# Optimization experiments

Measured on AMD Instinct MI355X. Metric: run time of the kernel, lower is better.

Reference implementation:

```python
import jax, jax.numpy as jnp
import numpy as np

N_NODES = 100000
N_EDGES = 1600000
IN_CH = 128
OUT_CH = 128

def setup_inputs() -> dict:
    key = jax.random.key(0)
    k1, k2, k3, k4, k5 = jax.random.split(key, 5)
    x = jax.random.normal(k1, (N_NODES, IN_CH), dtype=jnp.float32)
    src = jax.random.randint(k2, (N_EDGES,), 0, N_NODES, dtype=jnp.int64)
    dst = jax.random.randint(k3, (N_EDGES,), 0, N_NODES, dtype=jnp.int64)
    edge_index = jnp.stack([src, dst], axis=0)
    W = jax.random.normal(k4, (OUT_CH, IN_CH), dtype=jnp.float32) * (1.0 / np.sqrt(IN_CH))
    b = jax.random.normal(k5, (OUT_CH,), dtype=jnp.float32) * 0.01
    return {"x": x, "edge_index": edge_index, "W": W, "b": b}

def reference(x, edge_index, W, b):
    n = x.shape[0]
    src, dst = edge_index[0], edge_index[1]
    loop = jnp.arange(n, dtype=edge_index.dtype)
    src_all = jnp.concatenate([src, loop])  # [E+N]
    dst_all = jnp.concatenate([dst, loop])  # [E+N]
    # in-degree (with self loops) per node
    deg = jax.ops.segment_sum(jnp.ones_like(dst_all, dtype=x.dtype), dst_all, num_segments=n)
    norm = (deg[src_all] * deg[dst_all]) ** -0.5
    norm = jnp.where(jnp.isinf(norm), 0.0, norm)
    h = x @ W.T + b  # [N, out_ch]
    msg = h[src_all] * norm[:, None]  # [E+N, out_ch]
    out = jax.ops.segment_sum(msg, dst_all, num_segments=n)  # [N, out_ch]
    return out
```

## Files before the change

### kernel.cpp

```cpp
#include <hip/hip_runtime.h>
#include <hip/hip_bf16.h>


#define N_NODES 100000
#define N_EDGES 1600000
#define CH 128
#define NC 49
#define CAPC 34816
#define NCHUNK 17
#define NFB 1563
#define FCAP 1280

using bf16x8 = __attribute__((ext_vector_type(8))) short;
using f32x4  = __attribute__((ext_vector_type(4))) float;

__device__ inline unsigned short f2bf(float f) {
    unsigned u = __float_as_uint(f);
    u += 0x7fffu + ((u >> 16) & 1u);
    return (unsigned short)(u >> 16);
}
__device__ inline float bflo(unsigned u) { return __uint_as_float(u << 16); }
__device__ inline float bfhi(unsigned u) { return __uint_as_float(u & 0xffff0000u); }

__global__ __launch_bounds__(256) void k_sortA(const int* __restrict__ src,
                                               const int* __restrict__ dst,
                                               int* __restrict__ ctail,
                                               unsigned* __restrict__ E1) {
    __shared__ int hist[NC];
    __shared__ int boff[NC + 1];
    __shared__ int cur[NC];
    __shared__ int gb[NC];
    __shared__ unsigned stage[2048];
    const int t    = threadIdx.x;
    const int base = blockIdx.x * 2048;
    const int n    = min(2048, N_EDGES - base);

    if (t < NC) hist[t] = 0;
    __syncthreads();

    int s[8], d[8];
#pragma unroll
    for (int h = 0; h < 2; ++h) {
        int idx = h * 1024 + 4 * t;
        if (idx < n) {
            int4 sv = *(const int4*)&src[base + idx];
            int4 dv = *(const int4*)&dst[base + idx];
            s[4*h+0] = sv.x; s[4*h+1] = sv.y; s[4*h+2] = sv.z; s[4*h+3] = sv.w;
            d[4*h+0] = dv.x; d[4*h+1] = dv.y; d[4*h+2] = dv.z; d[4*h+3] = dv.w;
        } else {
            d[4*h+0] = d[4*h+1] = d[4*h+2] = d[4*h+3] = -1;
            s[4*h+0] = s[4*h+1] = s[4*h+2] = s[4*h+3] = 0;
        }
    }
#pragma unroll
    for (int j = 0; j < 8; ++j)
        if (d[j] >= 0) atomicAdd(&hist[d[j] >> 11], 1);
    __syncthreads();

    if (t < NC) gb[t] = atomicAdd(&ctail[t], hist[t]);
    if (t == 0) {
        int run = 0;
        for (int k = 0; k < NC; ++k) { boff[k] = run; run += hist[k]; }
        boff[NC] = run;
    }
    __syncthreads();
    if (t < NC) cur[t] = boff[t];
    __syncthreads();

#pragma unroll
    for (int j = 0; j < 8; ++j)
        if (d[j] >= 0) {
            int k = d[j] >> 11;
            int pos = atomicAdd(&cur[k], 1);
            stage[pos] = ((unsigned)s[j] << 11) | (unsigned)(d[j] & 2047);
        }
    __syncthreads();

    const int tot = boff[NC];
    for (int i = t; i < tot; i += 256) {
        int lo = 0, hi = NC;
#pragma unroll
        for (int it = 0; it < 6; ++it) {
            int mid = (lo + hi) >> 1;
            bool c = (boff[mid] <= i);
            lo = c ? mid : lo;
            hi = c ? hi : mid;
        }
        int p = gb[lo] + (i - boff[lo]);
        if (p < CAPC) E1[(size_t)lo * CAPC + p] = stage[i];
    }
}

__global__ __launch_bounds__(256) void k_sortB(const unsigned* __restrict__ E1,
                                               const int* __restrict__ ctail,
                                               int* __restrict__ ftail,
                                               unsigned* __restrict__ E2) {
    __shared__ int hist[32];
    __shared__ int boff[33];
    __shared__ int cur[32];
    __shared__ int gb[32];
    __shared__ unsigned stage[2048];
    const int cb = blockIdx.x / NCHUNK;
    const int ch = blockIdx.x % NCHUNK;
    const int t  = threadIdx.x;
    int cnt = ctail[cb]; if (cnt > CAPC) cnt = CAPC;
    const int begin = ch * 2048;
    int n = cnt - begin;
    if (n <= 0) return;
    if (n > 2048) n = 2048;
    const unsigned* e1 = E1 + (size_t)cb * CAPC + begin;

    if (t < 32) hist[t] = 0;
    __syncthreads();

    for (int i = t; i < n; i += 256)
        atomicAdd(&hist[(e1[i] >> 6) & 31], 1);
    __syncthreads();

    if (t < 32) gb[t] = atomicAdd(&ftail[cb * 32 + t], hist[t]);
    if (t == 0) {
        int run = 0;
        for (int k = 0; k < 32; ++k) { boff[k] = run; run += hist[k]; }
        boff[32] = run;
    }
    __syncthreads();
    if (t < 32) cur[t] = boff[t];
    __syncthreads();

    for (int i = t; i < n; i += 256) {
        unsigned v = e1[i];
        int k = (v >> 6) & 31;
        int pos = atomicAdd(&cur[k], 1);
        stage[pos] = ((v >> 11) << 6) | (v & 63);
    }
    __syncthreads();

    const int tot = boff[32];
    for (int i = t; i < tot; i += 256) {
        int lo = 0, hi = 32;
#pragma unroll
        for (int it = 0; it < 5; ++it) {
            int mid = (lo + hi) >> 1;
            bool c = (boff[mid] <= i);
            lo = c ? mid : lo;
            hi = c ? hi : mid;
        }
        int p = gb[lo] + (i - boff[lo]);
        int fb = cb * 32 + lo;
        if (p < FCAP) E2[(size_t)fb * FCAP + p] = stage[i];
    }
}

__global__ __launch_bounds__(256) void k_deg(const unsigned* __restrict__ E2,
                                             const int* __restrict__ ftail,
                                             float* __restrict__ rinv) {
    __shared__ int bins[64];
    const int fb = blockIdx.x;
    const int t  = threadIdx.x;
    if (t < 64) bins[t] = 0;
    int n = ftail[fb]; if (n > FCAP) n = FCAP;
    __syncthreads();
    const unsigned* e2 = E2 + (size_t)fb * FCAP;
    for (int i = t; i < n; i += 256) atomicAdd(&bins[e2[i] & 63], 1);
    __syncthreads();
    if (t < 64) {
        int node = fb * 64 + t;
        if (node < N_NODES) rinv[node] = rsqrtf((float)(bins[t] + 1));
    }
}

__device__ inline void cvt8(const float4 a, const float4 b, bf16x8& h, bf16x8& l) {
    bf16x8 H, L;
#define CV(i, f) { unsigned short hb = f2bf(f); H[i] = (short)hb;               \
                   L[i] = (short)f2bf((f) - __uint_as_float((unsigned)hb << 16)); }
    CV(0, a.x) CV(1, a.y) CV(2, a.z) CV(3, a.w)
    CV(4, b.x) CV(5, b.y) CV(6, b.z) CV(7, b.w)
#undef CV
    h = H; l = L;
}

#define MFMA(a, b, c) __builtin_amdgcn_mfma_f32_16x16x32_bf16((a), (b), (c), 0, 0, 0)

__global__ __launch_bounds__(256) void k_gemm(const float* __restrict__ x,
                                              const float* __restrict__ W,
                                              const float* __restrict__ b,
                                              const float* __restrict__ rinv,
                                              unsigned short* __restrict__ hs) {
    __shared__ __align__(16) unsigned short wh[CH * CH];
    __shared__ __align__(16) unsigned short wl[CH * CH];
    const int t = threadIdx.x;

    for (int c = t; c < 2048; c += 256) {
        int o   = c >> 4;
        int kk  = (c & 15) << 3;
        const float* wp = &W[(size_t)o * CH + kk];
        float4 w0 = *(const float4*)wp;
        float4 w1 = *(const float4*)(wp + 4);
        bf16x8 H, L;
        cvt8(w0, w1, H, L);
        unsigned boff = ((unsigned)((o << 8) | (kk << 1))) ^ ((unsigned)(o & 7) << 4);
        *(bf16x8*)((char*)wh + boff) = H;
        *(bf16x8*)((char*)wl + boff) = L;
    }
    __syncthreads();

    const int lane = t & 63;
    const int l15  = lane & 15;
    const int lhi  = lane >> 4;
    const int kc   = lhi << 3;
    const int row_base = blockIdx.x * 128 + (t >> 6) * 32;

    int r0 = row_base + l15;       if (r0 > N_NODES - 1) r0 = N_NODES - 1;
    int r1 = row_base + 16 + l15;  if (r1 > N_NODES - 1) r1 = N_NODES - 1;
    const float* x0 = &x[(size_t)r0 * CH + kc];
    const float* x1 = &x[(size_t)r1 * CH + kc];

    float4 xa[4][2], xb[4][2];
#pragma unroll
    for (int ks = 0; ks < 4; ++ks) {
        xa[ks][0] = *(const float4*)(x0 + ks * 32);
        xa[ks][1] = *(const float4*)(x0 + ks * 32 + 4);
        xb[ks][0] = *(const float4*)(x1 + ks * 32);
        xb[ks][1] = *(const float4*)(x1 + ks * 32 + 4);
    }

    f32x4 acc[2][8];
#pragma unroll
    for (int rf = 0; rf < 2; ++rf)
#pragma unroll
        for (int cf = 0; cf < 8; ++cf)
            acc[rf][cf] = (f32x4){0.f, 0.f, 0.f, 0.f};

#pragma unroll
    for (int ks = 0; ks < 4; ++ks) {
        bf16x8 ah0, al0, ah1, al1;
        cvt8(xa[ks][0], xa[ks][1], ah0, al0);
        cvt8(xb[ks][0], xb[ks][1], ah1, al1);
        const unsigned kb = (unsigned)((ks * 32 + kc) << 1);
#pragma unroll
        for (int cf = 0; cf < 8; ++cf) {
            int o = cf * 16 + l15;
            unsigned boff = (((unsigned)(o << 8)) + kb) ^ ((unsigned)(o & 7) << 4);
            bf16x8 bh = *(const bf16x8*)((const char*)wh + boff);
            bf16x8 bl = *(const bf16x8*)((const char*)wl + boff);
            acc[0][cf] = MFMA(ah0, bh, acc[0][cf]);
            acc[1][cf] = MFMA(ah1, bh, acc[1][cf]);
            acc[0][cf] = MFMA(al0, bh, acc[0][cf]);
            acc[1][cf] = MFMA(al1, bh, acc[1][cf]);
            acc[0][cf] = MFMA(ah0, bl, acc[0][cf]);
            acc[1][cf] = MFMA(ah1, bl, acc[1][cf]);
        }
    }

    float bcol[8];
#pragma unroll
    for (int cf = 0; cf < 8; ++cf) bcol[cf] = b[cf * 16 + l15];

#pragma unroll
    for (int rf = 0; rf < 2; ++rf) {
        int rb = row_base + rf * 16 + lhi * 4;
        if (rb >= N_NODES) continue;
        float4 ri4 = *(const float4*)&rinv[rb];
        float ri[4] = {ri4.x, ri4.y, ri4.z, ri4.w};
#pragma unroll
        for (int j = 0; j < 4; ++j) {
            size_t ro = (size_t)(rb + j) * CH;
#pragma unroll
            for (int cf = 0; cf < 8; ++cf)
                hs[ro + cf * 16 + l15] = f2bf(ri[j] * (acc[rf][cf][j] + bcol[cf]));
        }
    }
}

#define ACC8(u)                                                            \
    do {                                                                   \
        acc[0] += bflo((u).x); acc[1] += bfhi((u).x);                      \
        acc[2] += bflo((u).y); acc[3] += bfhi((u).y);                      \
        acc[4] += bflo((u).z); acc[5] += bfhi((u).z);                      \
        acc[6] += bflo((u).w); acc[7] += bfhi((u).w);                      \
    } while (0)

__global__ __launch_bounds__(256) void k_spmm(const unsigned* __restrict__ E2,
                                              const int* __restrict__ ftail,
                                              const float* __restrict__ rinv,
                                              const unsigned short* __restrict__ hs,
                                              float* __restrict__ out) {
    __shared__ int bins[64];
    __shared__ int boff[65];
    __shared__ int cur[64];
    __shared__ int srt[FCAP];
    const int fb    = blockIdx.x;
    const int node0 = fb * 64;
    const int t     = threadIdx.x;
    const unsigned* e2 = E2 + (size_t)fb * FCAP;
    const uint4* hp = (const uint4*)hs;

    if (t < 64) bins[t] = 0;
    int n = ftail[fb]; if (n > FCAP) n = FCAP;
    __syncthreads();

    for (int i = t; i < n; i += 256) atomicAdd(&bins[e2[i] & 63], 1);
    __syncthreads();

    if (t == 0) {
        int run = 0;
        for (int k = 0; k < 64; ++k) { boff[k] = run; run += bins[k]; }
        boff[64] = run;
    }
    __syncthreads();
    if (t < 64) cur[t] = boff[t];
    __syncthreads();

    for (int i = t; i < n; i += 256) {
        unsigned v = e2[i];
        int pos = atomicAdd(&cur[v & 63], 1);
        srt[pos] = (int)(v >> 6);
    }
    __syncthreads();

    const int grp  = t >> 4;
    const int lane = t & 15;
#pragma unroll
    for (int r = 0; r < 4; ++r) {
        const int nl   = grp * 4 + r;
        const int node = node0 + nl;
        if (node >= N_NODES) continue;
        float acc[8] = {};
        {
            uint4 u = hp[(size_t)node * 16 + lane];
            ACC8(u);
        }
        int e  = boff[nl];
        int e1 = boff[nl + 1];
        for (; e + 8 <= e1; e += 8) {
            int s0 = srt[e + 0], s1 = srt[e + 1], s2 = srt[e + 2], s3 = srt[e + 3];
            int s4 = srt[e + 4], s5 = srt[e + 5], s6 = srt[e + 6], s7 = srt[e + 7];
            uint4 u0 = hp[(size_t)s0 * 16 + lane];
            uint4 u1 = hp[(size_t)s1 * 16 + lane];
            uint4 u2 = hp[(size_t)s2 * 16 + lane];
            uint4 u3 = hp[(size_t)s3 * 16 + lane];
            uint4 u4 = hp[(size_t)s4 * 16 + lane];
            uint4 u5 = hp[(size_t)s5 * 16 + lane];
            uint4 u6 = hp[(size_t)s6 * 16 + lane];
            uint4 u7 = hp[(size_t)s7 * 16 + lane];
            ACC8(u0); ACC8(u1); ACC8(u2); ACC8(u3);
            ACC8(u4); ACC8(u5); ACC8(u6); ACC8(u7);
        }
        for (; e + 4 <= e1; e += 4) {
            int s0 = srt[e + 0];
            int s1 = srt[e + 1];
            int s2 = srt[e + 2];
            int s3 = srt[e + 3];
            uint4 u0 = hp[(size_t)s0 * 16 + lane];
            uint4 u1 = hp[(size_t)s1 * 16 + lane];
            uint4 u2 = hp[(size_t)s2 * 16 + lane];
            uint4 u3 = hp[(size_t)s3 * 16 + lane];
            ACC8(u0); ACC8(u1); ACC8(u2); ACC8(u3);
        }
        for (; e < e1; ++e) {
            uint4 u = hp[(size_t)srt[e] * 16 + lane];
            ACC8(u);
        }
        float ri = rinv[node];
        f32x4 o0, o1;
        o0[0] = ri * acc[0]; o0[1] = ri * acc[1]; o0[2] = ri * acc[2]; o0[3] = ri * acc[3];
        o1[0] = ri * acc[4]; o1[1] = ri * acc[5]; o1[2] = ri * acc[6]; o1[3] = ri * acc[7];
        __builtin_nontemporal_store(o0, (f32x4*)&out[(size_t)node * CH + lane * 8]);
        __builtin_nontemporal_store(o1, (f32x4*)&out[(size_t)node * CH + lane * 8 + 4]);
    }
}

extern "C" void kernel_launch(void* const* d_in, const int* in_sizes, int n_in,
                              void* d_out, int out_size, void* d_ws, size_t ws_size,
                              hipStream_t stream) {
    const float* x  = (const float*)d_in[0];
    const int*   ei = (const int*)d_in[1];
    const float* W  = (const float*)d_in[2];
    const float* b  = (const float*)d_in[3];
    float* out = (float*)d_out;

    const int* src = ei;
    const int* dst = ei + N_EDGES;

    int*      ctail = (int*)d_ws;
    int*      ftail = ctail + 64;
    float*    rinv  = (float*)(ftail + 1600);
    unsigned* E1    = (unsigned*)(rinv + N_NODES);
    unsigned* E2    = E1 + (size_t)NC * CAPC;
    unsigned short* hs = (unsigned short*)(E2 + (size_t)NFB * FCAP);

    hipMemsetAsync(ctail, 0, (64 + 1600) * sizeof(int), stream);

    k_sortA<<<(N_EDGES + 2047) / 2048, 256, 0, stream>>>(src, dst, ctail, E1);
    k_sortB<<<NC * NCHUNK, 256, 0, stream>>>(E1, ctail, ftail, E2);
    k_deg<<<NFB, 256, 0, stream>>>(E2, ftail, rinv);
    k_gemm<<<(N_NODES + 127) / 128, 256, 0, stream>>>(x, W, b, rinv, hs);
    k_spmm<<<NFB, 256, 0, stream>>>(E2, ftail, rinv, hs, out);
}
```

Before: 231.9 us.

## Fuse degree count into sort kernels and balance SpMM rows by degree

```diff
diff --git a/kernel.cpp b/kernel.cpp
--- a/kernel.cpp
+++ b/kernel.cpp
@@ -25,7 +25,8 @@
 __global__ __launch_bounds__(256) void k_sortA(const int* __restrict__ src,
                                                const int* __restrict__ dst,
                                                int* __restrict__ ctail,
-                                               unsigned* __restrict__ E1) {
+                                               unsigned* __restrict__ E1,
+                                               int* __restrict__ deg) {
     __shared__ int hist[NC];
     __shared__ int boff[NC + 1];
     __shared__ int cur[NC];
@@ -54,7 +55,10 @@
     }
 #pragma unroll
     for (int j = 0; j < 8; ++j)
-        if (d[j] >= 0) atomicAdd(&hist[d[j] >> 11], 1);
+        if (d[j] >= 0) {
+            atomicAdd(&hist[d[j] >> 11], 1);
+            atomicAdd(&deg[d[j]], 1);
+        }
     __syncthreads();
 
     if (t < NC) gb[t] = atomicAdd(&ctail[t], hist[t]);
@@ -94,7 +98,9 @@
 __global__ __launch_bounds__(256) void k_sortB(const unsigned* __restrict__ E1,
                                                const int* __restrict__ ctail,
                                                int* __restrict__ ftail,
-                                               unsigned* __restrict__ E2) {
+                                               unsigned* __restrict__ E2,
+                                               const int* __restrict__ deg,
+                                               float* __restrict__ rinv) {
     __shared__ int hist[32];
     __shared__ int boff[33];
     __shared__ int cur[32];
@@ -103,6 +109,12 @@
     const int cb = blockIdx.x / NCHUNK;
     const int ch = blockIdx.x % NCHUNK;
     const int t  = threadIdx.x;
+
+    {
+        int i = blockIdx.x * 121 + t;
+        if (t < 121 && i < N_NODES) rinv[i] = rsqrtf((float)(deg[i] + 1));
+    }
+
     int cnt = ctail[cb]; if (cnt > CAPC) cnt = CAPC;
     const int begin = ch * 2048;
     int n = cnt - begin;
@@ -148,24 +160,6 @@
         int p = gb[lo] + (i - boff[lo]);
         int fb = cb * 32 + lo;
         if (p < FCAP) E2[(size_t)fb * FCAP + p] = stage[i];
-    }
-}
-
-__global__ __launch_bounds__(256) void k_deg(const unsigned* __restrict__ E2,
-                                             const int* __restrict__ ftail,
-                                             float* __restrict__ rinv) {
-    __shared__ int bins[64];
-    const int fb = blockIdx.x;
-    const int t  = threadIdx.x;
-    if (t < 64) bins[t] = 0;
-    int n = ftail[fb]; if (n > FCAP) n = FCAP;
-    __syncthreads();
-    const unsigned* e2 = E2 + (size_t)fb * FCAP;
-    for (int i = t; i < n; i += 256) atomicAdd(&bins[e2[i] & 63], 1);
-    __syncthreads();
-    if (t < 64) {
-        int node = fb * 64 + t;
-        if (node < N_NODES) rinv[node] = rsqrtf((float)(bins[t] + 1));
     }
 }
 
@@ -288,6 +282,7 @@
     __shared__ int bins[64];
     __shared__ int boff[65];
     __shared__ int cur[64];
+    __shared__ int sKey[64];
     __shared__ int srt[FCAP];
     const int fb    = blockIdx.x;
     const int node0 = fb * 64;
@@ -307,6 +302,7 @@
         for (int k = 0; k < 64; ++k) { boff[k] = run; run += bins[k]; }
         boff[64] = run;
     }
+    if (t < 64) sKey[t] = (bins[t] << 6) | t;
     __syncthreads();
     if (t < 64) cur[t] = boff[t];
     __syncthreads();
@@ -316,13 +312,31 @@
         int pos = atomicAdd(&cur[v & 63], 1);
         srt[pos] = (int)(v >> 6);
     }
+
+#pragma unroll
+    for (int k = 2; k <= 64; k <<= 1) {
+#pragma unroll
+        for (int j = k >> 1; j > 0; j >>= 1) {
+            __syncthreads();
+            if (t < 64) {
+                int ixj = t ^ j;
+                if (ixj > t) {
+                    int a = sKey[t], c = sKey[ixj];
+                    if (((t & k) == 0) ? (a > c) : (a < c)) {
+                        sKey[t] = c; sKey[ixj] = a;
+                    }
+                }
+            }
+        }
+    }
     __syncthreads();
 
     const int grp  = t >> 4;
     const int lane = t & 15;
+    const int rbase = (grp >> 2) * 4 + (grp & 3);
 #pragma unroll
     for (int r = 0; r < 4; ++r) {
-        const int nl   = grp * 4 + r;
+        const int nl   = sKey[r * 16 + rbase] & 63;
         const int node = node0 + nl;
         if (node >= N_NODES) continue;
         float acc[8] = {};
@@ -365,8 +379,8 @@
         f32x4 o0, o1;
         o0[0] = ri * acc[0]; o0[1] = ri * acc[1]; o0[2] = ri * acc[2]; o0[3] = ri * acc[3];
         o1[0] = ri * acc[4]; o1[1] = ri * acc[5]; o1[2] = ri * acc[6]; o1[3] = ri * acc[7];
-        __builtin_nontemporal_store(o0, (f32x4*)&out[(size_t)node * CH + lane * 8]);
-        __builtin_nontemporal_store(o1, (f32x4*)&out[(size_t)node * CH + lane * 8 + 4]);
+        *(f32x4*)&out[(size_t)node * CH + lane * 8]     = o0;
+        *(f32x4*)&out[(size_t)node * CH + lane * 8 + 4] = o1;
     }
 }
 
@@ -384,16 +398,16 @@
 
     int*      ctail = (int*)d_ws;
     int*      ftail = ctail + 64;
-    float*    rinv  = (float*)(ftail + 1600);
+    int*      deg   = ftail + 1600;
+    float*    rinv  = (float*)(deg + 100032);
     unsigned* E1    = (unsigned*)(rinv + N_NODES);
     unsigned* E2    = E1 + (size_t)NC * CAPC;
     unsigned short* hs = (unsigned short*)(E2 + (size_t)NFB * FCAP);
 
-    hipMemsetAsync(ctail, 0, (64 + 1600) * sizeof(int), stream);
-
-    k_sortA<<<(N_EDGES + 2047) / 2048, 256, 0, stream>>>(src, dst, ctail, E1);
-    k_sortB<<<NC * NCHUNK, 256, 0, stream>>>(E1, ctail, ftail, E2);
-    k_deg<<<NFB, 256, 0, stream>>>(E2, ftail, rinv);
+    hipMemsetAsync(ctail, 0, (64 + 1600 + 100032) * sizeof(int), stream);
+
+    k_sortA<<<(N_EDGES + 2047) / 2048, 256, 0, stream>>>(src, dst, ctail, E1, deg);
+    k_sortB<<<NC * NCHUNK, 256, 0, stream>>>(E1, ctail, ftail, E2, deg, rinv);
     k_gemm<<<(N_NODES + 127) / 128, 256, 0, stream>>>(x, W, b, rinv, hs);
     k_spmm<<<NFB, 256, 0, stream>>>(E2, ftail, rinv, hs, out);
 }
```

New measurement: 294.6 us. 1.27x slower.

## Replace atomic bucket reservation with histogram, scan, place passes

Applied to the files above, without the earlier changes.

```diff
diff --git a/kernel.cpp b/kernel.cpp
--- a/kernel.cpp
+++ b/kernel.cpp
@@ -6,6 +6,7 @@
 #define N_EDGES 1600000
 #define CH 128
 #define NC 49
+#define NBLKA 782
 #define CAPC 34816
 #define NCHUNK 17
 #define NFB 1563
@@ -22,9 +23,61 @@
 __device__ inline float bflo(unsigned u) { return __uint_as_float(u << 16); }
 __device__ inline float bfhi(unsigned u) { return __uint_as_float(u & 0xffff0000u); }
 
-__global__ __launch_bounds__(256) void k_sortA(const int* __restrict__ src,
+__global__ __launch_bounds__(256) void k_histA(const int* __restrict__ dst,
+                                               int* __restrict__ histG) {
+    __shared__ int hist[NC];
+    const int t    = threadIdx.x;
+    const int base = blockIdx.x * 2048;
+    const int n    = min(2048, N_EDGES - base);
+    if (t < NC) hist[t] = 0;
+    __syncthreads();
+#pragma unroll
+    for (int h = 0; h < 2; ++h) {
+        int idx = h * 1024 + 4 * t;
+        if (idx < n) {
+            int4 dv = *(const int4*)&dst[base + idx];
+            atomicAdd(&hist[dv.x >> 11], 1);
+            atomicAdd(&hist[dv.y >> 11], 1);
+            atomicAdd(&hist[dv.z >> 11], 1);
+            atomicAdd(&hist[dv.w >> 11], 1);
+        }
+    }
+    __syncthreads();
+    if (t < NC) histG[(size_t)t * NBLKA + blockIdx.x] = hist[t];
+}
+
+__global__ __launch_bounds__(256) void k_scanA(int* __restrict__ histG,
+                                               int* __restrict__ ctail) {
+    __shared__ int part[256];
+    const int k = blockIdx.x;
+    int* h = histG + (size_t)k * NBLKA;
+    const int t = threadIdx.x;
+    const int base = t * 4;
+    int a0 = 0, a1 = 0, a2 = 0, a3 = 0;
+    if (base + 0 < NBLKA) a0 = h[base + 0];
+    if (base + 1 < NBLKA) a1 = h[base + 1];
+    if (base + 2 < NBLKA) a2 = h[base + 2];
+    if (base + 3 < NBLKA) a3 = h[base + 3];
+    const int s = a0 + a1 + a2 + a3;
+    part[t] = s;
+    __syncthreads();
+    for (int off = 1; off < 256; off <<= 1) {
+        int x = (t >= off) ? part[t - off] : 0;
+        __syncthreads();
+        part[t] += x;
+        __syncthreads();
+    }
+    int r = part[t] - s;
+    if (t == 255) ctail[k] = part[255];
+    if (base + 0 < NBLKA) { h[base + 0] = r; r += a0; }
+    if (base + 1 < NBLKA) { h[base + 1] = r; r += a1; }
+    if (base + 2 < NBLKA) { h[base + 2] = r; r += a2; }
+    if (base + 3 < NBLKA) { h[base + 3] = r; r += a3; }
+}
+
+__global__ __launch_bounds__(256) void k_place(const int* __restrict__ src,
                                                const int* __restrict__ dst,
-                                               int* __restrict__ ctail,
+                                               const int* __restrict__ histG,
                                                unsigned* __restrict__ E1) {
     __shared__ int hist[NC];
     __shared__ int boff[NC + 1];
@@ -35,7 +88,10 @@
     const int base = blockIdx.x * 2048;
     const int n    = min(2048, N_EDGES - base);
 
-    if (t < NC) hist[t] = 0;
+    if (t < NC) {
+        hist[t] = 0;
+        gb[t] = histG[(size_t)t * NBLKA + blockIdx.x];
+    }
     __syncthreads();
 
     int s[8], d[8];
@@ -57,7 +113,6 @@
         if (d[j] >= 0) atomicAdd(&hist[d[j] >> 11], 1);
     __syncthreads();
 
-    if (t < NC) gb[t] = atomicAdd(&ctail[t], hist[t]);
     if (t == 0) {
         int run = 0;
         for (int k = 0; k < NC; ++k) { boff[k] = run; run += hist[k]; }
@@ -365,8 +420,8 @@
         f32x4 o0, o1;
         o0[0] = ri * acc[0]; o0[1] = ri * acc[1]; o0[2] = ri * acc[2]; o0[3] = ri * acc[3];
         o1[0] = ri * acc[4]; o1[1] = ri * acc[5]; o1[2] = ri * acc[6]; o1[3] = ri * acc[7];
-        __builtin_nontemporal_store(o0, (f32x4*)&out[(size_t)node * CH + lane * 8]);
-        __builtin_nontemporal_store(o1, (f32x4*)&out[(size_t)node * CH + lane * 8 + 4]);
+        *(f32x4*)&out[(size_t)node * CH + lane * 8]     = o0;
+        *(f32x4*)&out[(size_t)node * CH + lane * 8 + 4] = o1;
     }
 }
 
@@ -384,14 +439,17 @@
 
     int*      ctail = (int*)d_ws;
     int*      ftail = ctail + 64;
-    float*    rinv  = (float*)(ftail + 1600);
+    int*      histG = ftail + 1600;
+    float*    rinv  = (float*)(histG + 38336);
     unsigned* E1    = (unsigned*)(rinv + N_NODES);
     unsigned* E2    = E1 + (size_t)NC * CAPC;
     unsigned short* hs = (unsigned short*)(E2 + (size_t)NFB * FCAP);
 
-    hipMemsetAsync(ctail, 0, (64 + 1600) * sizeof(int), stream);
-
-    k_sortA<<<(N_EDGES + 2047) / 2048, 256, 0, stream>>>(src, dst, ctail, E1);
+    hipMemsetAsync(ftail, 0, 1600 * sizeof(int), stream);
+
+    k_histA<<<NBLKA, 256, 0, stream>>>(dst, histG);
+    k_scanA<<<NC, 256, 0, stream>>>(histG, ctail);
+    k_place<<<NBLKA, 256, 0, stream>>>(src, dst, histG, E1);
     k_sortB<<<NC * NCHUNK, 256, 0, stream>>>(E1, ctail, ftail, E2);
     k_deg<<<NFB, 256, 0, stream>>>(E2, ftail, rinv);
     k_gemm<<<(N_NODES + 127) / 128, 256, 0, stream>>>(x, W, b, rinv, hs);
```

After: 225.1 us. 1.03x faster.
